# Kernel tuning notes

Hardware: AMD Instinct MI355X
Metric: run time of the kernel (lower is better)

Reference implementation:

```python
import jax, jax.numpy as jnp
import numpy as np

CODEBOOK_SIZE = 1024
LATENT_DIM = 64
BETA = 0.25

def setup_inputs() -> dict:
    key = jax.random.key(0)
    k1, k2 = jax.random.split(key)
    B, C, T = 32, LATENT_DIM, 4096
    x = jax.random.normal(k1, (B, C, T), dtype=jnp.float32)
    # codebook initialized uniform(-1/K, 1/K) as in the torch module
    emb = jax.random.uniform(k2, (CODEBOOK_SIZE, LATENT_DIM), dtype=jnp.float32,
                             minval=-1.0 / CODEBOOK_SIZE, maxval=1.0 / CODEBOOK_SIZE)
    return {"x": x, "emb": emb}

def reference(x, emb):
    B, C, T = x.shape  # C == LATENT_DIM
    xf = jnp.transpose(x, (0, 2, 1)).reshape(B * T, C)  # [BT, D]
    d = (jnp.sum(xf * xf, axis=-1, keepdims=True)
         + jnp.sum(emb * emb, axis=-1)[None, :]
         - 2.0 * jnp.matmul(xf, emb.T))  # [BT, K]
    idx = jnp.argmin(d, axis=-1)  # [BT] int
    q = emb[idx].reshape(B, T, C).transpose(0, 2, 1)  # [B, C, T]
    commitment_loss = BETA * jnp.mean((jax.lax.stop_gradient(q) - x) ** 2)
    codebook_loss = jnp.mean((q - jax.lax.stop_gradient(x)) ** 2)
    quant_out = x + jax.lax.stop_gradient(q - x)  # straight-through
    return quant_out, codebook_loss, commitment_loss, idx.reshape(B, T)
```

## Files before the change

### kernel.cpp

```cpp
#include <hip/hip_runtime.h>


typedef unsigned long long u64;
typedef unsigned short u16;
typedef __attribute__((ext_vector_type(8))) short bf8_t;
typedef __attribute__((ext_vector_type(4))) float f4_t;

#define KCB 1024
#define DD 64
#define BB 32
#define TT 4096
#define BT (BB * TT)
#define NELEM (BB * DD * TT)

#define RPB 128
#define NT 16
#define FB_MAX 48
#define BAND 4e-5f

#define WS_LOSS 0
#define WS_E2 64
#define WS_EH 2048
#define WS_EL 34816

static __device__ __forceinline__ u16 bf16rte(float f) {
    unsigned u = __float_as_uint(f);
    return (u16)((u + 0x7FFFu + ((u >> 16) & 1u)) >> 16);
}
static __device__ __forceinline__ unsigned flipf(float f) {
    unsigned u = __float_as_uint(f);
    return (u & 0x80000000u) ? ~u : (u | 0x80000000u);
}
static __device__ __forceinline__ int fragidx(int n, int d) {
    return 1024 * (n >> 4) + 512 * (d >> 5) + 128 * ((d >> 3) & 3)
         + 8 * (n & 15) + (d & 7);
}
static __device__ __forceinline__ void gload_lds16(const void* g, void* l) {
    __builtin_amdgcn_global_load_lds(
        (const __attribute__((address_space(1))) void*)g,
        (__attribute__((address_space(3))) void*)l, 16, 0, 0);
}

__global__ void vq_prep(const float* __restrict__ emb, float* __restrict__ ws) {
#pragma clang fp contract(off)
    const int tid = threadIdx.x;
    const int kl = tid >> 6, d = tid & 63;
    const int k = blockIdx.x * 4 + kl;
    if (blockIdx.x == 0 && tid == 0) ws[WS_LOSS] = 0.0f;
    __shared__ float sq[4][64];
    __shared__ float rsh[4][8];
    float v = emb[(size_t)k * DD + d];
    u16 hb = bf16rte(v);
    float hv = __uint_as_float((unsigned)hb << 16);
    u16 lb = bf16rte(v - hv);
    u16* ehg = (u16*)(ws + WS_EH) + 4096 * (k >> 6);
    u16* elg = (u16*)(ws + WS_EL) + 4096 * (k >> 6);
    const int ia = fragidx(k & 63, d);
    ehg[ia] = hb; elg[ia] = lb;
    sq[kl][d] = v * v;
    __syncthreads();
    if (tid < 32) {
        const int g = tid >> 3, j = tid & 7;
        float r = sq[g][j];
#pragma unroll
        for (int i = 1; i < 8; ++i) r += sq[g][8 * i + j];
        rsh[g][j] = r;
    }
    __syncthreads();
    if (tid < 4) {
        const float* r = rsh[tid];
        ws[WS_E2 + blockIdx.x * 4 + tid] =
            ((r[0] + r[1]) + (r[2] + r[3])) + ((r[4] + r[5]) + (r[6] + r[7]));
    }
}

__launch_bounds__(256, 4)
__global__ void vq_main(const float* __restrict__ x, const float* __restrict__ emb,
                        float* __restrict__ out, float* __restrict__ ws) {
#pragma clang fp contract(off)
    const int tid = threadIdx.x;
    const int lane = tid & 63;
    const int w = __builtin_amdgcn_readfirstlane(tid >> 6);
    const int l15 = lane & 15, q = lane >> 4;

    const int row0 = blockIdx.x * RPB;
    const int b = row0 >> 12;
    const int t0 = row0 & (TT - 1);

    __shared__ __align__(16) char arena[32768];
    u16* xhT = (u16*)arena;
    u16* xlT = (u16*)(arena + 16384);
    float* efs = (float*)arena;
    float* xfb = (float*)(arena + 16640);

    __shared__ float e2l[KCB];
    __shared__ float Srow[RPB];
    __shared__ int kwin[RPB];
    __shared__ int fbrows[FB_MAX];
    __shared__ int fbcnt;
    __shared__ float bsum;

    if (tid == 0) { fbcnt = 0; bsum = 0.0f; }
#pragma unroll
    for (int i = tid; i < KCB; i += 256) e2l[i] = ws[WS_E2 + i];

    if (tid < RPB) {
        const int r = tid;
        const float* xr = x + (size_t)b * DD * TT + t0 + r;
        const int gb = 1024 * (r >> 4);
        float rr[8];
#pragma unroll
        for (int i = 0; i < 64; i += 8) {
#pragma unroll
            for (int j = 0; j < 8; ++j) {
                float v = xr[(size_t)(i + j) * TT];
                if (i == 0) rr[j] = v * v; else rr[j] += v * v;
                u16 hb = bf16rte(v);
                float hv = __uint_as_float((unsigned)hb << 16);
                u16 lb = bf16rte(v - hv);
                const int ia = gb + fragidx(r & 15, i + j);
                xhT[ia] = hb; xlT[ia] = lb;
            }
        }
        Srow[r] = ((rr[0] + rr[1]) + (rr[2] + rr[3])) + ((rr[4] + rr[5]) + (rr[6] + rr[7]));
    }
    __syncthreads();

    bf8_t ah[2][2], al[2][2];
#pragma unroll
    for (int g = 0; g < 2; ++g) {
        const int gg = 2 * w + g;
        ah[g][0] = *(const bf8_t*)&xhT[1024 * gg + 8 * lane];
        ah[g][1] = *(const bf8_t*)&xhT[1024 * gg + 512 + 8 * lane];
        al[g][0] = *(const bf8_t*)&xlT[1024 * gg + 8 * lane];
        al[g][1] = *(const bf8_t*)&xlT[1024 * gg + 512 + 8 * lane];
    }
    float Sv[8];
#pragma unroll
    for (int g = 0; g < 2; ++g)
#pragma unroll
        for (int rg = 0; rg < 4; ++rg)
            Sv[4 * g + rg] = Srow[32 * w + 16 * g + 4 * q + rg];

    float v1[8], v2[8], kf[8];
#pragma unroll
    for (int s = 0; s < 8; ++s) { v1[s] = 3.4e38f; v2[s] = 3.4e38f; kf[s] = 0.0f; }

    const u16* ehg = (const u16*)(ws + WS_EH);
    const u16* elg = (const u16*)(ws + WS_EL);

    auto kstep = [&](float e2v, float kcol,
                     bf8_t bh0, bf8_t bl0, bf8_t bh1, bf8_t bl1) {
#pragma unroll
        for (int g = 0; g < 2; ++g) {
            f4_t acc = (f4_t){0.f, 0.f, 0.f, 0.f};
            acc = __builtin_amdgcn_mfma_f32_16x16x32_bf16(ah[g][0], bh0, acc, 0, 0, 0);
            acc = __builtin_amdgcn_mfma_f32_16x16x32_bf16(ah[g][0], bl0, acc, 0, 0, 0);
            acc = __builtin_amdgcn_mfma_f32_16x16x32_bf16(al[g][0], bh0, acc, 0, 0, 0);
            acc = __builtin_amdgcn_mfma_f32_16x16x32_bf16(ah[g][1], bh1, acc, 0, 0, 0);
            acc = __builtin_amdgcn_mfma_f32_16x16x32_bf16(ah[g][1], bl1, acc, 0, 0, 0);
            acc = __builtin_amdgcn_mfma_f32_16x16x32_bf16(al[g][1], bh1, acc, 0, 0, 0);
#pragma unroll
            for (int rg = 0; rg < 4; ++rg) {
                const int s = 4 * g + rg;
                float ck = Sv[s] + e2v;
                float u = __builtin_fmaf(-2.0f, acc[rg], ck);
                bool lt = u < v1[s];
                float sp = lt ? v1[s] : u;
                v2[s] = fminf(v2[s], sp);
                kf[s] = lt ? kcol : kf[s];
                v1[s] = fminf(v1[s], u);
            }
        }
    };

    const u16* psrc = (w < 2) ? ehg : elg;
    const int poff = (w & 1) * 512;
    char* const pdst0 = arena + 1024 * w;
    auto issue = [&](int it2, int bufi) {
        gload_lds16(psrc + 1024 * it2 + poff + 8 * lane, pdst0 + 4096 * bufi);
    };

    __syncthreads();
    issue(0, 0);
    issue(1, 1);
    asm volatile("s_waitcnt vmcnt(1)" ::: "memory");
    __builtin_amdgcn_s_barrier();
#pragma unroll 3
    for (int it = 0; it < 60; ++it) {
        const int cur = it % 3;
        const u16* bb = (const u16*)(arena + 4096 * cur);
        bf8_t bh0 = *(const bf8_t*)&bb[8 * lane];
        bf8_t bh1 = *(const bf8_t*)&bb[512 + 8 * lane];
        bf8_t bl0 = *(const bf8_t*)&bb[1024 + 8 * lane];
        bf8_t bl1 = *(const bf8_t*)&bb[1536 + 8 * lane];
        const float e2v = e2l[16 * it + l15];
        asm volatile("s_waitcnt lgkmcnt(0)" ::: "memory");
        __builtin_amdgcn_sched_barrier(0);
        issue(it + 2, (it + 2) % 3);
        kstep(e2v, (float)(16 * it + l15), bh0, bl0, bh1, bl1);
        asm volatile("s_waitcnt vmcnt(1)" ::: "memory");
        __builtin_amdgcn_s_barrier();
    }
#pragma unroll 1
    for (int it = 60; it < 64; ++it) {
        const int cur = it % 3;
        const u16* bb = (const u16*)(arena + 4096 * cur);
        bf8_t bh0 = *(const bf8_t*)&bb[8 * lane];
        bf8_t bh1 = *(const bf8_t*)&bb[512 + 8 * lane];
        bf8_t bl0 = *(const bf8_t*)&bb[1024 + 8 * lane];
        bf8_t bl1 = *(const bf8_t*)&bb[1536 + 8 * lane];
        const float e2v = e2l[16 * it + l15];
        asm volatile("s_waitcnt lgkmcnt(0)" ::: "memory");
        __builtin_amdgcn_sched_barrier(0);
        if (it < 62) issue(it + 2, (it + 2) % 3);
        kstep(e2v, (float)(16 * it + l15), bh0, bl0, bh1, bl1);
        if (it < 62) {
            asm volatile("s_waitcnt vmcnt(1)" ::: "memory");
        } else {
            asm volatile("s_waitcnt vmcnt(0)" ::: "memory");
        }
        __builtin_amdgcn_s_barrier();
    }

#pragma unroll
    for (int m = 1; m < 16; m <<= 1) {
#pragma unroll
        for (int s = 0; s < 8; ++s) {
            float ov1 = __shfl_xor(v1[s], m, 16);
            float okf = __shfl_xor(kf[s], m, 16);
            float ov2 = __shfl_xor(v2[s], m, 16);
            float nmx = fmaxf(v1[s], ov1);
            v2[s] = fminf(fminf(v2[s], ov2), nmx);
            bool lt = ov1 < v1[s];
            kf[s] = lt ? okf : kf[s];
            v1[s] = fminf(v1[s], ov1);
        }
    }
    if (l15 == 0) {
#pragma unroll
        for (int g = 0; g < 2; ++g)
#pragma unroll
            for (int rg = 0; rg < 4; ++rg) {
                const int s = 4 * g + rg;
                const int r = 32 * w + 16 * g + 4 * q + rg;
                kwin[r] = (int)kf[s];
                if (v2[s] <= v1[s] + BAND) {
                    int i = atomicAdd(&fbcnt, 1);
                    if (i < FB_MAX) fbrows[i] = r;
                }
            }
    }
    __syncthreads();

    const int cnt = min(fbcnt, FB_MAX);
    if (cnt > 0) {
        for (int i = tid; i < cnt * 64; i += 256) {
            int fi = i >> 6, l = i & 63;
            xfb[fi * 65 + l] = x[(size_t)b * DD * TT + (size_t)l * TT + t0 + fbrows[fi]];
        }
        u64 pmin[12];
#pragma unroll
        for (int sl = 0; sl < 12; ++sl) pmin[sl] = ~0ull;
#pragma unroll 1
        for (int T2 = 0; T2 < NT; ++T2) {
            __syncthreads();
            {
                const int n = tid >> 2, qd = (tid & 3) * 16;
                const float* sp = emb + (size_t)(T2 * 64 + n) * DD + qd;
                float* dp = efs + n * 65 + qd;
#pragma unroll
                for (int j = 0; j < 16; ++j) dp[j] = sp[j];
            }
            __syncthreads();
#pragma unroll
            for (int sl = 0; sl < 12; ++sl) {
                const int fi = w + 4 * sl;
                if (fi < cnt) {
                    float acc = 0.0f;
#pragma unroll
                    for (int i = 0; i < 64; ++i)
                        acc = __builtin_fmaf(efs[lane * 65 + i], xfb[fi * 65 + i], acc);
                    float ck = Srow[fbrows[fi]] + e2l[T2 * 64 + lane];
                    float u = __builtin_fmaf(-2.0f, acc, ck);
                    u64 pk = ((u64)flipf(u) << 10) | (unsigned)(T2 * 64 + lane);
                    pmin[sl] = pmin[sl] < pk ? pmin[sl] : pk;
                }
            }
        }
#pragma unroll
        for (int sl = 0; sl < 12; ++sl) {
            const int fi = w + 4 * sl;
            if (fi < cnt) {
                u64 pk = pmin[sl];
#pragma unroll
                for (int dl = 32; dl > 0; dl >>= 1) {
                    u64 o = __shfl_xor(pk, dl);
                    pk = o < pk ? o : pk;
                }
                if (lane == 0) kwin[fbrows[fi]] = (int)(pk & 1023u);
            }
        }
        __syncthreads();
    }

    if (tid < RPB) out[NELEM + 2 + row0 + tid] = (float)kwin[tid];

    const int r = tid & 127, c0 = (tid >> 7) * 32;
    const int kw = kwin[r];
    const float* eqr = emb + (size_t)kw * DD;
    float lsum = 0.0f;
#pragma unroll 8
    for (int i = 0; i < 32; ++i) {
        const int c = c0 + i;
        const size_t o = (size_t)b * DD * TT + (size_t)c * TT + t0 + r;
        float qv = eqr[c];
        float xv = x[o];
        out[o] = qv;
        float a = qv - xv;
        lsum = __builtin_fmaf(a, a, lsum);
    }
#pragma unroll
    for (int off = 32; off > 0; off >>= 1) lsum += __shfl_down(lsum, off);
    if (lane == 0) atomicAdd(&bsum, lsum);
    __syncthreads();
    if (tid == 0) atomicAdd(ws + WS_LOSS, bsum);
}

__global__ void vq_finalize(const float* __restrict__ ws, float* __restrict__ out) {
    if (threadIdx.x == 0 && blockIdx.x == 0) {
        float M = ws[WS_LOSS] / (float)NELEM;
        out[NELEM + 0] = M;
        out[NELEM + 1] = 0.25f * M;
    }
}

extern "C" void kernel_launch(void* const* d_in, const int* in_sizes, int n_in,
                              void* d_out, int out_size, void* d_ws, size_t ws_size,
                              hipStream_t stream) {
    const float* x = (const float*)d_in[0];
    const float* emb = (const float*)d_in[1];
    float* out = (float*)d_out;
    float* ws = (float*)d_ws;

    vq_prep<<<KCB / 4, 256, 0, stream>>>(emb, ws);
    vq_main<<<BT / RPB, 256, 0, stream>>>(x, emb, out, ws);
    vq_finalize<<<1, 64, 0, stream>>>(ws, out);
}
```

Before: 198.3 us.

## Batch codebook LDS prefetch into double-buffered groups of four steps

The main loop used a three-slot ring with one global-to-LDS prefetch, a wait and a workgroup barrier per 16-column step. Now each prefetch fills a group of four steps, double-buffered in two 16 KB halves, so there is one wait and one barrier per four steps. This is meant to cut barrier and wait overhead and give the MFMA work longer uninterrupted stretches. In exchange it needs more LDS, which could lower occupancy or overflow the arena if that was not sized for it, and it uses a coarser vmcnt(0) wait instead of keeping one load in flight.

```diff
diff --git a/kernel.cpp b/kernel.cpp
--- a/kernel.cpp
+++ b/kernel.cpp
@@ -176,51 +176,38 @@
 
     const u16* psrc = (w < 2) ? ehg : elg;
     const int poff = (w & 1) * 512;
-    char* const pdst0 = arena + 1024 * w;
-    auto issue = [&](int it2, int bufi) {
-        gload_lds16(psrc + 1024 * it2 + poff + 8 * lane, pdst0 + 4096 * bufi);
+    auto issue_group = [&](int gg) {
+#pragma unroll
+        for (int j = 0; j < 4; ++j) {
+            const int t = 4 * gg + j;
+            gload_lds16(psrc + 1024 * t + poff + 8 * lane,
+                        arena + 16384 * ((t >> 2) & 1) + 4096 * j + 1024 * w);
+        }
     };
 
     __syncthreads();
-    issue(0, 0);
-    issue(1, 1);
-    asm volatile("s_waitcnt vmcnt(1)" ::: "memory");
+    issue_group(0);
+    asm volatile("s_waitcnt vmcnt(0)" ::: "memory");
     __builtin_amdgcn_s_barrier();
-#pragma unroll 3
-    for (int it = 0; it < 60; ++it) {
-        const int cur = it % 3;
-        const u16* bb = (const u16*)(arena + 4096 * cur);
-        bf8_t bh0 = *(const bf8_t*)&bb[8 * lane];
-        bf8_t bh1 = *(const bf8_t*)&bb[512 + 8 * lane];
-        bf8_t bl0 = *(const bf8_t*)&bb[1024 + 8 * lane];
-        bf8_t bl1 = *(const bf8_t*)&bb[1536 + 8 * lane];
-        const float e2v = e2l[16 * it + l15];
-        asm volatile("s_waitcnt lgkmcnt(0)" ::: "memory");
+    __builtin_amdgcn_sched_barrier(0);
+    issue_group(1);
+#pragma unroll 1
+    for (int g = 0; g < 16; ++g) {
+        const char* gbuf = arena + 16384 * (g & 1);
+#pragma unroll
+        for (int j = 0; j < 4; ++j) {
+            const int it = 4 * g + j;
+            const u16* bb = (const u16*)(gbuf + 4096 * j);
+            bf8_t bh0 = *(const bf8_t*)&bb[8 * lane];
+            bf8_t bh1 = *(const bf8_t*)&bb[512 + 8 * lane];
+            bf8_t bl0 = *(const bf8_t*)&bb[1024 + 8 * lane];
+            bf8_t bl1 = *(const bf8_t*)&bb[1536 + 8 * lane];
+            kstep(e2l[16 * it + l15], (float)(16 * it + l15), bh0, bl0, bh1, bl1);
+        }
+        asm volatile("s_waitcnt vmcnt(0)" ::: "memory");
+        __builtin_amdgcn_s_barrier();
         __builtin_amdgcn_sched_barrier(0);
-        issue(it + 2, (it + 2) % 3);
-        kstep(e2v, (float)(16 * it + l15), bh0, bl0, bh1, bl1);
-        asm volatile("s_waitcnt vmcnt(1)" ::: "memory");
-        __builtin_amdgcn_s_barrier();
-    }
-#pragma unroll 1
-    for (int it = 60; it < 64; ++it) {
-        const int cur = it % 3;
-        const u16* bb = (const u16*)(arena + 4096 * cur);
-        bf8_t bh0 = *(const bf8_t*)&bb[8 * lane];
-        bf8_t bh1 = *(const bf8_t*)&bb[512 + 8 * lane];
-        bf8_t bl0 = *(const bf8_t*)&bb[1024 + 8 * lane];
-        bf8_t bl1 = *(const bf8_t*)&bb[1536 + 8 * lane];
-        const float e2v = e2l[16 * it + l15];
-        asm volatile("s_waitcnt lgkmcnt(0)" ::: "memory");
-        __builtin_amdgcn_sched_barrier(0);
-        if (it < 62) issue(it + 2, (it + 2) % 3);
-        kstep(e2v, (float)(16 * it + l15), bh0, bl0, bh1, bl1);
-        if (it < 62) {
-            asm volatile("s_waitcnt vmcnt(1)" ::: "memory");
-        } else {
-            asm volatile("s_waitcnt vmcnt(0)" ::: "memory");
-        }
-        __builtin_amdgcn_s_barrier();
+        if (g < 14) issue_group(g + 2);
     }
 
 #pragma unroll
```

Result: faster. 193.6 us (-2.4%).
